# Kernel tuning notes

Hardware: AMD Instinct MI355X
Metric: run time of the kernel (lower is better)

## Reference

```python
import jax, jax.numpy as jnp
import numpy as np
from jax import lax

D_MODEL, D_STATE, D_CONV, EXPAND = 768, 16, 4, 2
D_INNER = EXPAND * D_MODEL          # 1536
DT_RANK = D_MODEL // 16             # 48
B_SZ, H_TOK, W_TOK = 2, 64, 32
L_SEQ = H_TOK * W_TOK               # 2048


def setup_inputs() -> dict:
    key = jax.random.key(0)
    ks = jax.random.split(key, 8)
    s = lambda k, shape: (jax.random.normal(k, shape, jnp.float32) * 0.02)
    A_log = jnp.log(jnp.tile(jnp.arange(1, D_STATE + 1, dtype=jnp.float32), (D_INNER, 1)))
    return {
        "x": jax.random.normal(ks[0], (B_SZ, L_SEQ, D_MODEL), jnp.float32),
        "ln_w": jnp.ones((D_MODEL,), jnp.float32),
        "ln_b": jnp.zeros((D_MODEL,), jnp.float32),
        "in_proj_w": s(ks[1], (2 * D_INNER, D_MODEL)),
        "conv_w": s(ks[2], (D_INNER, 1, D_CONV)),   # depthwise kernel [O, I/g=1, K]
        "conv_b": jnp.zeros((D_INNER,), jnp.float32),
        "x_proj_w": s(ks[3], (DT_RANK + 2 * D_STATE, D_INNER)),
        "dt_proj_w": s(ks[4], (D_INNER, DT_RANK)),
        "dt_proj_b": 0.01 * jax.random.normal(ks[5], (D_INNER,), jnp.float32),
        "A_log": A_log,
        "D_param": jnp.ones((D_INNER,), jnp.float32),
        "out_proj_w": s(ks[6], (D_MODEL, D_INNER)),
        "H": H_TOK,
        "W": W_TOK,
    }


def _layernorm(x, w, b, eps=1e-5):
    mu = jnp.mean(x, axis=-1, keepdims=True)
    var = jnp.mean(jnp.square(x - mu), axis=-1, keepdims=True)
    return (x - mu) * lax.rsqrt(var + eps) * w + b


def _mamba_forward(xn, in_proj_w, conv_w, conv_b, x_proj_w, dt_proj_w, dt_proj_b, A_log, D_param, out_proj_w):
    # in_proj and split into x / z gates, both [B, L, d_inner]
    xz = jnp.einsum('bld,ed->ble', xn, in_proj_w)
    x_in, z = jnp.split(xz, 2, axis=-1)

    # causal depthwise conv1d over time
    x_ch = jnp.transpose(x_in, (0, 2, 1))  # [B, d_inner, L]
    x_ch = lax.conv_general_dilated(
        x_ch, conv_w, window_strides=(1,), padding=[(D_CONV - 1, 0)],
        dimension_numbers=('NCH', 'OIH', 'NCH'), feature_group_count=D_INNER)
    x_ch = x_ch + conv_b[None, :, None]
    x_s = jax.nn.silu(jnp.transpose(x_ch, (0, 2, 1)))  # [B, L, d_inner]

    # input-dependent dt, B, C
    x_dbl = jnp.einsum('bld,ed->ble', x_s, x_proj_w)
    dt = x_dbl[..., :DT_RANK]
    B_ssm = x_dbl[..., DT_RANK:DT_RANK + D_STATE]      # [B, L, N]
    C_ssm = x_dbl[..., DT_RANK + D_STATE:]             # [B, L, N]
    dt = jax.nn.softplus(jnp.einsum('blr,dr->bld', dt, dt_proj_w) + dt_proj_b)  # [B, L, d_inner]

    A = -jnp.exp(A_log)                                # [d_inner, N]
    deltaA = jnp.exp(dt[..., None] * A)                # [B, L, d_inner, N]
    deltaBu = dt[..., None] * B_ssm[:, :, None, :] * x_s[..., None]

    def step(h, inputs):
        dA_t, dBu_t, c_t = inputs
        h = dA_t * h + dBu_t                           # [B, d_inner, N]
        y_t = jnp.einsum('bdn,bn->bd', h, c_t)
        return h, y_t

    h0 = jnp.zeros((xn.shape[0], D_INNER, D_STATE), xn.dtype)
    _, ys = lax.scan(step, h0, (jnp.transpose(deltaA, (1, 0, 2, 3)),
                                jnp.transpose(deltaBu, (1, 0, 2, 3)),
                                jnp.transpose(C_ssm, (1, 0, 2))))
    y = jnp.transpose(ys, (1, 0, 2)) + x_s * D_param   # skip via D
    y = y * jax.nn.silu(z)
    return jnp.einsum('ble,de->bld', y, out_proj_w)


def reference(x, ln_w, ln_b, in_proj_w, conv_w, conv_b, x_proj_w, dt_proj_w, dt_proj_b, A_log, D_param, out_proj_w, H, W):
    xn = _layernorm(x, ln_w, ln_b)
    out = _mamba_forward(xn, in_proj_w, conv_w, conv_b, x_proj_w, dt_proj_w, dt_proj_b, A_log, D_param, out_proj_w)
    return out
```

## Files before the change

### kernel.cpp

```cpp
#include <hip/hip_runtime.h>

#define DM   768
#define DI   1536
#define DS   16
#define DTR  48
#define BSZ  2
#define LSEQ 2048
#define BL   (BSZ*LSEQ)
#define NC   64
#define CL   (LSEQ/NC)
#define LOG2E 1.4426950408889634f
#define RLOG2E 0.6931471805599453f

typedef short bf16x8 __attribute__((ext_vector_type(8)));
typedef short short8 __attribute__((ext_vector_type(8)));
typedef float f32x4  __attribute__((ext_vector_type(4)));

static __device__ __forceinline__ unsigned short f2bf(float f){
  union { float f; unsigned u; } v; v.f = f;
  unsigned r = v.u + 0x7FFFu + ((v.u >> 16) & 1u);
  return (unsigned short)(r >> 16);
}
static __device__ __forceinline__ float bf2f(unsigned short s){
  union { unsigned u; float f; } v; v.u = ((unsigned)s) << 16;
  return v.f;
}
static __device__ __forceinline__ unsigned short f2h(float f){
  union { _Float16 h; unsigned short u; } v; v.h = (_Float16)f; return v.u;
}
static __device__ __forceinline__ float h2f(unsigned short u){
  union { unsigned short u; _Float16 h; } v; v.u = u; return (float)v.h;
}
static __device__ __forceinline__ float fexp2(float x){ return __builtin_amdgcn_exp2f(x); }
static __device__ __forceinline__ float flog2(float x){ return __builtin_amdgcn_logf(x); }
static __device__ __forceinline__ float frcp(float x){ return __builtin_amdgcn_rcpf(x); }

static __device__ __forceinline__ void gload_lds16(const unsigned short* g, unsigned short* l){
  __builtin_amdgcn_global_load_lds(
      (const __attribute__((address_space(1))) void*)g,
      (__attribute__((address_space(3))) void*)l, 16, 0, 0);
}

#define EE0 (3072*768)
#define EE1 (EE0 + 128*1536)
#define EE2 (EE1 + 1536*64)
#define EE3 (EE2 + 768*1536)
#define NPAD ((EE3 + 255)/256)
__global__ __launch_bounds__(256) void pad_ln(const float* __restrict__ s0,
    const float* __restrict__ s1, const float* __restrict__ s2, const float* __restrict__ s3,
    unsigned short* __restrict__ d0, unsigned short* __restrict__ d1,
    unsigned short* __restrict__ d2, unsigned short* __restrict__ d3,
    const float* __restrict__ x, const float* __restrict__ lw,
    const float* __restrict__ lb, unsigned short* __restrict__ xn){
  __shared__ float ls_[4], lss_[4];
  if (blockIdx.x < NPAD){
    int idx = blockIdx.x*256 + threadIdx.x;
    if (idx < EE0){
      d0[idx] = f2bf(s0[idx]);
    } else if (idx < EE1){
      int i = idx - EE0; int n = i / 1536, k = i % 1536;
      d1[i] = (n < 80) ? f2bf(s1[(size_t)n*1536 + k]) : (unsigned short)0;
    } else if (idx < EE2){
      int i = idx - EE1; int n = i >> 6, k = i & 63;
      d2[i] = (k < DTR) ? f2bf(s2[(size_t)n*DTR + k]) : (unsigned short)0;
    } else if (idx < EE3){
      int i = idx - EE2;
      d3[i] = f2bf(s3[i]);
    }
    return;
  }
  int row = blockIdx.x - NPAD;
  const float* xr = x + (size_t)row*DM;
  float v[3]; float s=0.f, ss=0.f;
#pragma unroll
  for (int i=0;i<3;i++){ v[i]=xr[threadIdx.x + i*256]; s+=v[i]; ss+=v[i]*v[i]; }
  for (int o=32;o>0;o>>=1){ s += __shfl_down(s,o); ss += __shfl_down(ss,o); }
  int wv = threadIdx.x>>6;
  if ((threadIdx.x&63)==0){ ls_[wv]=s; lss_[wv]=ss; }
  __syncthreads();
  s  = ls_[0]+ls_[1]+ls_[2]+ls_[3];
  ss = lss_[0]+lss_[1]+lss_[2]+lss_[3];
  float mu  = s*(1.f/DM);
  float var = ss*(1.f/DM) - mu*mu;
  float rs  = rsqrtf(var + 1e-5f);
#pragma unroll
  for (int i=0;i<3;i++){
    int j = threadIdx.x + i*256;
    xn[(size_t)row*DM + j] = f2bf((v[i]-mu)*rs*lw[j] + lb[j]);
  }
}

__global__ __launch_bounds__(512) void gemm256(const unsigned short* __restrict__ A,
    const unsigned short* __restrict__ W, unsigned short* __restrict__ outS0,
    unsigned short* __restrict__ outS1)
{
  const int K = DM;
  __shared__ unsigned short As[3][8192];
  __shared__ unsigned short Ws[3][8192];
  const int tid = threadIdx.x, lane = tid & 63, wave = tid >> 6;
  const int wm = wave >> 2, wn = wave & 3;
  const int m0 = blockIdx.y*256, n0 = blockIdx.x*256;
  const int srow = lane >> 2;
  const int gch  = (lane & 3) ^ (srow & 3);
  const unsigned short* gA0 = A + (size_t)(m0 + wave*16 + srow)*K + gch*8;
  const unsigned short* gW0 = W + (size_t)(n0 + wave*16 + srow)*K + gch*8;
  const int lo0 = (wave*64)*8;
  const int r = lane & 15, kb = lane >> 4;

  f32x4 acc[8][4];
#pragma unroll
  for (int i=0;i<8;i++)
#pragma unroll
    for (int j=0;j<4;j++){ f32x4 zv = {0.f,0.f,0.f,0.f}; acc[i][j] = zv; }

  int fAo[8], fWo[4];
#pragma unroll
  for (int mi=0;mi<8;mi++){ int rr = wm*128 + mi*16 + r; fAo[mi] = (rr*4 + (kb ^ (rr&3)))*8; }
#pragma unroll
  for (int ni=0;ni<4;ni++){ int rw = wn*64 + ni*16 + r; fWo[ni] = (rw*4 + (kb ^ (rw&3)))*8; }

  gload_lds16(gA0,                    &As[0][lo0]);
  gload_lds16(gA0 + (size_t)128*K,    &As[0][lo0 + 4096]);
  gload_lds16(gW0,                    &Ws[0][lo0]);
  gload_lds16(gW0 + (size_t)128*K,    &Ws[0][lo0 + 4096]);

  const int nt = K >> 5;
  int cur = 0, nxt = 1;
  for (int t=0; t<nt; ++t){
    if (t+1 < nt){
      const int ko = (t+1)*32;
      gload_lds16(gA0 + ko,                 &As[nxt][lo0]);
      gload_lds16(gA0 + ko + (size_t)128*K, &As[nxt][lo0 + 4096]);
      gload_lds16(gW0 + ko,                 &Ws[nxt][lo0]);
      gload_lds16(gW0 + ko + (size_t)128*K, &Ws[nxt][lo0 + 4096]);
      asm volatile("s_waitcnt vmcnt(4)" ::: "memory");
    } else {
      asm volatile("s_waitcnt vmcnt(0)" ::: "memory");
    }
    __builtin_amdgcn_s_barrier();
    __builtin_amdgcn_sched_barrier(0);
    bf16x8 af[8], bw[4];
#pragma unroll
    for (int i=0;i<8;i++) af[i] = *(const bf16x8*)(&As[cur][0] + fAo[i]);
#pragma unroll
    for (int i=0;i<4;i++) bw[i] = *(const bf16x8*)(&Ws[cur][0] + fWo[i]);
#pragma unroll
    for (int mi=0;mi<8;mi++)
#pragma unroll
      for (int ni=0;ni<4;ni++)
        acc[mi][ni] = __builtin_amdgcn_mfma_f32_16x16x32_bf16(af[mi], bw[ni], acc[mi][ni], 0,0,0);
    cur = nxt;
    nxt = (nxt == 2) ? 0 : nxt + 1;
  }
  const int cr = (lane>>4)*4, cc = lane & 15;
#pragma unroll
  for (int mi=0;mi<8;mi++)
#pragma unroll
  for (int ni=0;ni<4;ni++)
#pragma unroll
  for (int j=0;j<4;j++){
    int m = m0 + wm*128 + mi*16 + cr + j;
    int n = n0 + wn*64 + ni*16 + cc;
    float cval = acc[mi][ni][j];
    if (n < DI){
      outS0[(size_t)m*DI + n] = f2bf(cval);
    } else {
      float sv = cval * frcp(1.f + fexp2(-cval*LOG2E));
      outS1[(size_t)m*DI + (n-DI)] = f2bf(sv);
    }
  }
}

__global__ __launch_bounds__(256) void gemm_lds(const unsigned short* __restrict__ A,
    const unsigned short* __restrict__ W, int K, float* __restrict__ outF)
{
  __shared__ unsigned short As[3][4096];
  __shared__ unsigned short Ws[3][4096];
  const int tid = threadIdx.x, lane = tid & 63, wave = tid >> 6;
  const int wm = wave >> 1, wn = wave & 1;
  const int m0 = blockIdx.y*128, n0 = blockIdx.x*128;
  const int srow = lane >> 2;
  const int gch  = (lane & 3) ^ (srow & 3);
  const unsigned short* gA0 = A + (size_t)(m0 + wave*16 + srow)*K + gch*8;
  const unsigned short* gW0 = W + (size_t)(n0 + wave*16 + srow)*K + gch*8;
  const int lo = wave*512;
  const int r = lane & 15, kb = lane >> 4;
  const int fx = (kb ^ (r & 3))*8;
  const int fAo = (wm*64 + r)*32 + fx;
  const int fWo = (wn*64 + r)*32 + fx;

  f32x4 acc[4][4];
#pragma unroll
  for (int i=0;i<4;i++)
#pragma unroll
    for (int j=0;j<4;j++){ f32x4 zv = {0.f,0.f,0.f,0.f}; acc[i][j] = zv; }

  gload_lds16(gA0,                &As[0][lo]);
  gload_lds16(gA0 + (size_t)64*K, &As[0][2048+lo]);
  gload_lds16(gW0,                &Ws[0][lo]);
  gload_lds16(gW0 + (size_t)64*K, &Ws[0][2048+lo]);

  const int nt = K >> 5;
  int cur = 0, nxt = 1;
  for (int t=0; t<nt; ++t){
    if (t+1 < nt){
      const int ko = (t+1)*32;
      gload_lds16(gA0 + ko,                &As[nxt][lo]);
      gload_lds16(gA0 + ko + (size_t)64*K, &As[nxt][2048+lo]);
      gload_lds16(gW0 + ko,                &Ws[nxt][lo]);
      gload_lds16(gW0 + ko + (size_t)64*K, &Ws[nxt][2048+lo]);
      asm volatile("s_waitcnt vmcnt(4)" ::: "memory");
    } else {
      asm volatile("s_waitcnt vmcnt(0)" ::: "memory");
    }
    __builtin_amdgcn_s_barrier();
    __builtin_amdgcn_sched_barrier(0);
    const unsigned short* fA = &As[cur][0] + fAo;
    const unsigned short* fW = &Ws[cur][0] + fWo;
    bf16x8 af[4], bw[4];
#pragma unroll
    for (int i=0;i<4;i++) af[i] = *(const bf16x8*)(fA + i*512);
#pragma unroll
    for (int i=0;i<4;i++) bw[i] = *(const bf16x8*)(fW + i*512);
#pragma unroll
    for (int mi=0;mi<4;mi++)
#pragma unroll
      for (int ni=0;ni<4;ni++)
        acc[mi][ni] = __builtin_amdgcn_mfma_f32_16x16x32_bf16(af[mi], bw[ni], acc[mi][ni], 0,0,0);
    cur = nxt;
    nxt = (nxt == 2) ? 0 : nxt + 1;
  }
  const int cr = (lane>>4)*4, cc = lane & 15;
#pragma unroll
  for (int mi=0;mi<4;mi++)
#pragma unroll
  for (int ni=0;ni<4;ni++)
#pragma unroll
  for (int j=0;j<4;j++){
    int m = m0 + wm*64 + mi*16 + cr + j;
    int n = n0 + wn*64 + ni*16 + cc;
    outF[(size_t)m*DM + n] = acc[mi][ni][j];
  }
}

__global__ __launch_bounds__(256) void gemm_xdt(const unsigned short* __restrict__ A,
    const unsigned short* __restrict__ W, const unsigned short* __restrict__ Wdt,
    const float* __restrict__ bias, float* __restrict__ outF,
    unsigned short* __restrict__ dt_h)
{
  __shared__ unsigned short dtt[16][72];
  const int K = DI;
  const int lane = threadIdx.x & 63, wave = threadIdx.x >> 6;
  const int m0 = blockIdx.x*16;
  const int n0 = wave*32;
  const int r = lane & 15, kb = lane >> 4;
  const unsigned short* Ap = A + (size_t)(m0 + r)*K + kb*8;
  const unsigned short* Wp = W + (size_t)(n0 + r)*K + kb*8;
  f32x4 acc[2];
#pragma unroll
  for (int j=0;j<2;j++){ f32x4 zv = {0.f,0.f,0.f,0.f}; acc[j] = zv; }
  for (int k=0;k<K;k+=32){
    bf16x8 af = *(const bf16x8*)(Ap + k);
    bf16x8 bw0 = *(const bf16x8*)(Wp + k);
    bf16x8 bw1 = *(const bf16x8*)(Wp + (size_t)16*K + k);
    acc[0] = __builtin_amdgcn_mfma_f32_16x16x32_bf16(af, bw0, acc[0], 0,0,0);
    acc[1] = __builtin_amdgcn_mfma_f32_16x16x32_bf16(af, bw1, acc[1], 0,0,0);
  }
  const int cr = (lane>>4)*4, cc = lane & 15;
#pragma unroll
  for (int ni=0;ni<2;ni++)
#pragma unroll
  for (int j=0;j<4;j++){
    int m = m0 + cr + j;
    int n = n0 + ni*16 + cc;
    float v = acc[ni][j];
    outF[(size_t)m*128 + n] = v;
    if (n < 64)
      dtt[cr+j][n] = (n < DTR) ? f2bf(v) : (unsigned short)0;
  }
  __syncthreads();
  bf16x8 af2[2];
#pragma unroll
  for (int s=0;s<2;s++) af2[s] = *(const bf16x8*)(&dtt[r][s*32 + kb*8]);
#pragma unroll
  for (int nf=0; nf<24; nf++){
    int nb = wave*384 + nf*16;
    const unsigned short* wp = Wdt + (size_t)(nb + r)*64 + kb*8;
    bf16x8 b0 = *(const bf16x8*)(wp);
    bf16x8 b1 = *(const bf16x8*)(wp + 32);
    f32x4 a2 = {0.f,0.f,0.f,0.f};
    a2 = __builtin_amdgcn_mfma_f32_16x16x32_bf16(af2[0], b0, a2, 0,0,0);
    a2 = __builtin_amdgcn_mfma_f32_16x16x32_bf16(af2[1], b1, a2, 0,0,0);
    int n = nb + cc;
    float bn = bias[n];
#pragma unroll
    for (int j=0;j<4;j++){
      float q = a2[j] + bn;
      float sp = flog2(1.f + fexp2(q*LOG2E)) * RLOG2E;
      dt_h[(size_t)(m0 + cr + j)*DI + n] = f2h(sp);
    }
  }
}

__global__ __launch_bounds__(192) void conv_silu(const unsigned short* __restrict__ x_in,
    const float* __restrict__ cw, const float* __restrict__ cb,
    unsigned short* __restrict__ xs)
{
  const int lb = (blockIdx.x & 511)*4;
  const int b  = blockIdx.x >> 9;
  const int d8 = threadIdx.x * 8;
  f32x4 w[8];
#pragma unroll
  for (int dd=0;dd<8;dd++) w[dd] = *(const f32x4*)(cw + (d8+dd)*4);
  float cbv[8];
  {
    f32x4 c0 = *(const f32x4*)(cb + d8);
    f32x4 c1 = *(const f32x4*)(cb + d8 + 4);
#pragma unroll
    for (int dd=0;dd<4;dd++){ cbv[dd]=c0[dd]; cbv[4+dd]=c1[dd]; }
  }
  float xr[7][8];
#pragma unroll
  for (int rr=0; rr<7; rr++){
    int ls = lb - 3 + rr;
    if (ls >= 0){
      short8 xv = *(const short8*)(x_in + ((size_t)b*LSEQ + ls)*DI + d8);
#pragma unroll
      for (int dd=0;dd<8;dd++) xr[rr][dd] = bf2f((unsigned short)xv[dd]);
    } else {
#pragma unroll
      for (int dd=0;dd<8;dd++) xr[rr][dd] = 0.f;
    }
  }
#pragma unroll
  for (int j=0;j<4;j++){
    short8 o;
#pragma unroll
    for (int dd=0;dd<8;dd++){
      float a = cbv[dd] + w[dd][0]*xr[j][dd] + w[dd][1]*xr[j+1][dd]
                        + w[dd][2]*xr[j+2][dd] + w[dd][3]*xr[j+3][dd];
      float sv = a * frcp(1.f + fexp2(-a*LOG2E));
      o[dd] = (short)f2bf(sv);
    }
    *(short8*)(xs + ((size_t)b*LSEQ + lb + j)*DI + d8) = o;
  }
}

__global__ __launch_bounds__(256) void scan_p1(const unsigned short* __restrict__ dt_h,
    const unsigned short* __restrict__ xs, const float* __restrict__ xdbl,
    float* __restrict__ S, float* __restrict__ Et)
{
  __shared__ unsigned int dxs[CL*64];
  __shared__ float Bs[CL][16];
  const int d0 = blockIdx.x*64, c = blockIdx.y, b = blockIdx.z;
  const int tid = threadIdx.x;
  const int l0 = c*CL;
  {
    int rr = tid >> 3, dcol = (tid & 7)*8;
    size_t g = ((size_t)b*LSEQ + l0 + rr)*DI + d0 + dcol;
    short8 dv = *(const short8*)(dt_h + g);
    short8 xv = *(const short8*)(xs + g);
    unsigned int* dst = &dxs[rr*64 + dcol];
#pragma unroll
    for (int j=0;j<8;j++)
      dst[j] = ((unsigned)(unsigned short)xv[j] << 16) | (unsigned short)dv[j];
  }
#pragma unroll
  for (int it=0; it<2; it++){
    int ii = it*256 + tid; int rr = ii >> 4, cc2 = ii & 15;
    Bs[rr][cc2] = xdbl[((size_t)b*LSEQ + l0 + rr)*128 + 48 + cc2];
  }
  __syncthreads();
  const int dloc = tid >> 2, ng = tid & 3;
  float h0=0.f, h1=0.f, h2=0.f, h3=0.f;
  float sdt = 0.f;
  for (int t=0;t<CL;t++){
    unsigned int pk = dxs[t*64 + dloc];
    float dtv = h2f((unsigned short)(pk & 0xFFFFu));
    float xsv = bf2f((unsigned short)(pk >> 16));
    sdt += dtv;
    float dx = dtv*xsv;
    float E  = fexp2(-dtv*LOG2E);
    float E2 = E*E, E4 = E2*E2, E8 = E4*E4;
    float Eg = 1.f;
    if (ng & 1) Eg = E4;
    if (ng & 2) Eg *= E8;
    float e0 = Eg*E, e1 = e0*E, e2 = e0*E2, e3 = e1*E2;
    f32x4 Bq = *(const f32x4*)(&Bs[t][ng*4]);
    h0 = e0*h0 + dx*Bq[0];
    h1 = e1*h1 + dx*Bq[1];
    h2 = e2*h2 + dx*Bq[2];
    h3 = e3*h3 + dx*Bq[3];
  }
  const size_t bd = (size_t)b*DI + d0 + dloc;
  f32x4 sv = {h0,h1,h2,h3};
  *(f32x4*)(S + (bd*NC + c)*DS + ng*4) = sv;
  if (ng == 0) Et[bd*NC + c] = fexp2(-sdt*LOG2E);
}

__global__ __launch_bounds__(256) void scan_comb(const float* __restrict__ S,
    const float* __restrict__ Et, float* __restrict__ Hs){
  const int bd = blockIdx.x;
  const int n = threadIdx.x & 15, co = threadIdx.x >> 4;
  const int m = n + 1;
  __shared__ float PsL[16][17], SsL[16][17];
  const float* Sp = S + (size_t)bd*NC*DS;
  const float* Ep = Et + (size_t)bd*NC;
  float p[4], s[4];
#pragma unroll
  for (int j=0;j<4;j++){
    int cc = co*4 + j;
    float E = Ep[cc];
    float E2=E*E, E4=E2*E2, E8=E4*E4, E16=E8*E8;
    float pw = ((m&1)?E:1.f);
    pw *= ((m&2)?E2:1.f);
    pw *= ((m&4)?E4:1.f);
    pw *= ((m&8)?E8:1.f);
    pw *= ((m&16)?E16:1.f);
    p[j] = pw;
    s[j] = Sp[cc*DS + n];
  }
  float Pa=1.f, Sa=0.f;
#pragma unroll
  for (int j=0;j<4;j++){ Sa = p[j]*Sa + s[j]; Pa *= p[j]; }
  PsL[n][co] = Pa; SsL[n][co] = Sa;
  __syncthreads();
  if (threadIdx.x < 16){
    int nn = threadIdx.x;
    float h = 0.f;
#pragma unroll
    for (int q=0;q<16;q++){
      float P = PsL[nn][q], Sv = SsL[nn][q];
      SsL[nn][q] = h;
      h = P*h + Sv;
    }
  }
  __syncthreads();
  float h = SsL[n][co];
  float* Hp = Hs + (size_t)bd*NC*DS;
#pragma unroll
  for (int j=0;j<4;j++){
    int cc = co*4 + j;
    Hp[cc*DS + n] = h;
    h = p[j]*h + s[j];
  }
}

__global__ __launch_bounds__(256) void scan_p2(const unsigned short* __restrict__ dt_h,
    const unsigned short* __restrict__ xs, const unsigned short* __restrict__ z_bf,
    const float* __restrict__ xdbl, const float* __restrict__ Dp,
    const float* __restrict__ Hs, unsigned short* __restrict__ y_bf)
{
  __shared__ unsigned int dxs[CL*64];
  __shared__ unsigned short zss[CL*64];
  __shared__ unsigned short ys[CL*64];
  __shared__ float Bs[CL][16];
  __shared__ float Cs[CL][16];
  const int d0 = blockIdx.x*64, c = blockIdx.y, b = blockIdx.z;
  const int tid = threadIdx.x;
  const int l0 = c*CL;
  {
    int rr = tid >> 3, dcol = (tid & 7)*8;
    size_t g = ((size_t)b*LSEQ + l0 + rr)*DI + d0 + dcol;
    short8 dv = *(const short8*)(dt_h + g);
    short8 xv = *(const short8*)(xs + g);
    *(short8*)(&zss[rr*64 + dcol]) = *(const short8*)(z_bf + g);
    unsigned int* dst = &dxs[rr*64 + dcol];
#pragma unroll
    for (int j=0;j<8;j++)
      dst[j] = ((unsigned)(unsigned short)xv[j] << 16) | (unsigned short)dv[j];
  }
#pragma unroll
  for (int it=0; it<2; it++){
    int ii = it*256 + tid; int rr = ii >> 4, cc2 = ii & 15;
    const float* xr = xdbl + ((size_t)b*LSEQ + l0 + rr)*128;
    Bs[rr][cc2] = xr[48+cc2];
    Cs[rr][cc2] = xr[64+cc2];
  }
  __syncthreads();
  const int dloc = tid >> 2, ng = tid & 3;
  const size_t bd = (size_t)b*DI + d0 + dloc;
  float h0,h1,h2,h3;
  {
    f32x4 hv = *(const f32x4*)(Hs + (bd*NC + c)*DS + ng*4);
    h0=hv[0]; h1=hv[1]; h2=hv[2]; h3=hv[3];
  }
  const float dpar = Dp[d0 + dloc];
  for (int t=0;t<CL;t++){
    unsigned int pk = dxs[t*64 + dloc];
    float dtv = h2f((unsigned short)(pk & 0xFFFFu));
    float xsv = bf2f((unsigned short)(pk >> 16));
    float dx = dtv*xsv;
    float E  = fexp2(-dtv*LOG2E);
    float E2 = E*E, E4 = E2*E2, E8 = E4*E4;
    float Eg = 1.f;
    if (ng & 1) Eg = E4;
    if (ng & 2) Eg *= E8;
    float e0 = Eg*E, e1 = e0*E, e2 = e0*E2, e3 = e1*E2;
    f32x4 Bq = *(const f32x4*)(&Bs[t][ng*4]);
    f32x4 Cq = *(const f32x4*)(&Cs[t][ng*4]);
    h0 = e0*h0 + dx*Bq[0];
    h1 = e1*h1 + dx*Bq[1];
    h2 = e2*h2 + dx*Bq[2];
    h3 = e3*h3 + dx*Bq[3];
    float y = (h0*Cq[0] + h1*Cq[1]) + (h2*Cq[2] + h3*Cq[3]);
    y += __shfl_xor(y, 1);
    y += __shfl_xor(y, 2);
    if (ng == 0){
      float sg = bf2f(zss[t*64 + dloc]);
      float yg = (y + xsv*dpar) * sg;
      ys[t*64 + dloc] = f2bf(yg);
    }
  }
  __syncthreads();
  {
    int fi = tid*8;
    int rr = fi >> 6, dcol = fi & 63;
    *(short8*)(y_bf + ((size_t)b*LSEQ + l0 + rr)*DI + d0 + dcol) = *(const short8*)(&ys[fi]);
  }
}

extern "C" void kernel_launch(void* const* d_in, const int* in_sizes, int n_in,
                              void* d_out, int out_size, void* d_ws, size_t ws_size,
                              hipStream_t stream) {
  const float* x       = (const float*)d_in[0];
  const float* ln_w    = (const float*)d_in[1];
  const float* ln_b    = (const float*)d_in[2];
  const float* in_w    = (const float*)d_in[3];
  const float* conv_w  = (const float*)d_in[4];
  const float* conv_b  = (const float*)d_in[5];
  const float* xproj_w = (const float*)d_in[6];
  const float* dt_w    = (const float*)d_in[7];
  const float* dt_b    = (const float*)d_in[8];
  const float* D_param = (const float*)d_in[10];
  const float* out_w   = (const float*)d_in[11];
  float* out = (float*)d_out;
  (void)in_sizes; (void)n_in; (void)out_size; (void)ws_size;

  char* ws = (char*)d_ws;
  size_t off = 0;
  auto alloc = [&](size_t bytes)->void*{
    void* p = ws + off; off += (bytes + 255) & ~(size_t)255; return p;
  };
  unsigned short* W_in  = (unsigned short*)alloc((size_t)3072*768*2);
  unsigned short* W_x   = (unsigned short*)alloc((size_t)128*1536*2);
  unsigned short* W_dt  = (unsigned short*)alloc((size_t)1536*64*2);
  unsigned short* W_out = (unsigned short*)alloc((size_t)768*1536*2);
  unsigned short* xn    = (unsigned short*)alloc((size_t)BL*DM*2);
  unsigned short* x_in  = (unsigned short*)alloc((size_t)BL*DI*2);
  unsigned short* z_bf  = (unsigned short*)alloc((size_t)BL*DI*2);
  unsigned short* xs    = (unsigned short*)alloc((size_t)BL*DI*2);
  unsigned short* dt_h  = (unsigned short*)alloc((size_t)BL*DI*2);
  float*          x_dbl = (float*)alloc((size_t)BL*128*4);
  float*          S     = (float*)alloc((size_t)BSZ*DI*NC*DS*4);
  float*          Hs    = (float*)alloc((size_t)BSZ*DI*NC*DS*4);
  float* Et = (float*)xn;
  unsigned short* y_bf = x_in;

  pad_ln<<<NPAD + BL, 256, 0, stream>>>(in_w, xproj_w, dt_w, out_w,
                                        W_in, W_x, W_dt, W_out, x, ln_w, ln_b, xn);

  gemm256<<<dim3(3072/256, BL/256), 512, 0, stream>>>(xn, W_in, x_in, z_bf);

  conv_silu<<<BL/4, 192, 0, stream>>>(x_in, conv_w, conv_b, xs);

  gemm_xdt<<<BL/16, 256, 0, stream>>>(xs, W_x, W_dt, dt_b, x_dbl, dt_h);

  scan_p1<<<dim3(DI/64, NC, BSZ), 256, 0, stream>>>(dt_h, xs, x_dbl, S, Et);
  scan_comb<<<BSZ*DI, 256, 0, stream>>>(S, Et, Hs);
  scan_p2<<<dim3(DI/64, NC, BSZ), 256, 0, stream>>>(dt_h, xs, z_bf, x_dbl, D_param, Hs, y_bf);

  gemm_lds<<<dim3(DM/128, BL/128), 256, 0, stream>>>(y_bf, W_out, 1536, out);
}
```

Measured before the change: 165.4 us.

## Fuse chunked scan passes into one kernel with decoupled look-back flags

Replaces the three-kernel chunked selective scan (local chunk pass, cross-chunk combine, second pass) with a single kernel. Each block publishes its chunk-local state and summed dt to a global aggregate buffer, raises an atomic flag, then spins on the flags of all earlier chunks and serially combines their states before running the output pass. This drops two launches and the reload of dt/xs/B from global memory, in exchange for spin-waiting that depends on earlier chunks being scheduled first. Later chunks redo up to 63 combine steps each, and a memset of the flags is added.

New measurement: 464.1 us. 181% more time.

```diff
diff --git a/kernel.cpp b/kernel.cpp
--- a/kernel.cpp
+++ b/kernel.cpp
@@ -9,6 +9,8 @@
 #define BL   (BSZ*LSEQ)
 #define NC   64
 #define CL   (LSEQ/NC)
+#define NDT  24
+#define NREC 1088
 #define LOG2E 1.4426950408889634f
 #define RLOG2E 0.6931471805599453f
 
@@ -346,13 +348,19 @@
   }
 }
 
-__global__ __launch_bounds__(256) void scan_p1(const unsigned short* __restrict__ dt_h,
-    const unsigned short* __restrict__ xs, const float* __restrict__ xdbl,
-    float* __restrict__ S, float* __restrict__ Et)
+__global__ __launch_bounds__(256) void scan_fused(const unsigned short* __restrict__ dt_h,
+    const unsigned short* __restrict__ xs, const unsigned short* __restrict__ z_bf,
+    const float* __restrict__ xdbl, const float* __restrict__ Dp,
+    float* __restrict__ agg, int* __restrict__ flags,
+    unsigned short* __restrict__ y_bf)
 {
   __shared__ unsigned int dxs[CL*64];
+  __shared__ unsigned short zss[CL*64];
+  __shared__ unsigned short ys[CL*64];
   __shared__ float Bs[CL][16];
-  const int d0 = blockIdx.x*64, c = blockIdx.y, b = blockIdx.z;
+  __shared__ float Cs[CL][16];
+  const int dtile = blockIdx.x, c = blockIdx.y, b = blockIdx.z;
+  const int d0 = dtile*64;
   const int tid = threadIdx.x;
   const int l0 = c*CL;
   {
@@ -360,6 +368,7 @@
     size_t g = ((size_t)b*LSEQ + l0 + rr)*DI + d0 + dcol;
     short8 dv = *(const short8*)(dt_h + g);
     short8 xv = *(const short8*)(xs + g);
+    *(short8*)(&zss[rr*64 + dcol]) = *(const short8*)(z_bf + g);
     unsigned int* dst = &dxs[rr*64 + dcol];
 #pragma unroll
     for (int j=0;j<8;j++)
@@ -368,12 +377,13 @@
 #pragma unroll
   for (int it=0; it<2; it++){
     int ii = it*256 + tid; int rr = ii >> 4, cc2 = ii & 15;
-    Bs[rr][cc2] = xdbl[((size_t)b*LSEQ + l0 + rr)*128 + 48 + cc2];
+    const float* xrp = xdbl + ((size_t)b*LSEQ + l0 + rr)*128;
+    Bs[rr][cc2] = xrp[48+cc2];
+    Cs[rr][cc2] = xrp[64+cc2];
   }
   __syncthreads();
   const int dloc = tid >> 2, ng = tid & 3;
-  float h0=0.f, h1=0.f, h2=0.f, h3=0.f;
-  float sdt = 0.f;
+  float h0=0.f, h1=0.f, h2=0.f, h3=0.f, sdt=0.f;
   for (int t=0;t<CL;t++){
     unsigned int pk = dxs[t*64 + dloc];
     float dtv = h2f((unsigned short)(pk & 0xFFFFu));
@@ -392,99 +402,41 @@
     h2 = e2*h2 + dx*Bq[2];
     h3 = e3*h3 + dx*Bq[3];
   }
-  const size_t bd = (size_t)b*DI + d0 + dloc;
-  f32x4 sv = {h0,h1,h2,h3};
-  *(f32x4*)(S + (bd*NC + c)*DS + ng*4) = sv;
-  if (ng == 0) Et[bd*NC + c] = fexp2(-sdt*LOG2E);
-}
-
-__global__ __launch_bounds__(256) void scan_comb(const float* __restrict__ S,
-    const float* __restrict__ Et, float* __restrict__ Hs){
-  const int bd = blockIdx.x;
-  const int n = threadIdx.x & 15, co = threadIdx.x >> 4;
-  const int m = n + 1;
-  __shared__ float PsL[16][17], SsL[16][17];
-  const float* Sp = S + (size_t)bd*NC*DS;
-  const float* Ep = Et + (size_t)bd*NC;
-  float p[4], s[4];
-#pragma unroll
-  for (int j=0;j<4;j++){
-    int cc = co*4 + j;
-    float E = Ep[cc];
-    float E2=E*E, E4=E2*E2, E8=E4*E4, E16=E8*E8;
-    float pw = ((m&1)?E:1.f);
-    pw *= ((m&2)?E2:1.f);
-    pw *= ((m&4)?E4:1.f);
-    pw *= ((m&8)?E8:1.f);
-    pw *= ((m&16)?E16:1.f);
-    p[j] = pw;
-    s[j] = Sp[cc*DS + n];
-  }
-  float Pa=1.f, Sa=0.f;
-#pragma unroll
-  for (int j=0;j<4;j++){ Sa = p[j]*Sa + s[j]; Pa *= p[j]; }
-  PsL[n][co] = Pa; SsL[n][co] = Sa;
+  {
+    float* rec = agg + ((size_t)(b*NC + c)*NDT + dtile)*NREC;
+    f32x4 sv = {h0,h1,h2,h3};
+    *(f32x4*)(rec + dloc*16 + ng*4) = sv;
+    if (ng == 0) rec[1024 + dloc] = sdt;
+  }
   __syncthreads();
-  if (threadIdx.x < 16){
-    int nn = threadIdx.x;
-    float h = 0.f;
-#pragma unroll
-    for (int q=0;q<16;q++){
-      float P = PsL[nn][q], Sv = SsL[nn][q];
-      SsL[nn][q] = h;
-      h = P*h + Sv;
-    }
-  }
-  __syncthreads();
-  float h = SsL[n][co];
-  float* Hp = Hs + (size_t)bd*NC*DS;
-#pragma unroll
-  for (int j=0;j<4;j++){
-    int cc = co*4 + j;
-    Hp[cc*DS + n] = h;
-    h = p[j]*h + s[j];
-  }
-}
-
-__global__ __launch_bounds__(256) void scan_p2(const unsigned short* __restrict__ dt_h,
-    const unsigned short* __restrict__ xs, const unsigned short* __restrict__ z_bf,
-    const float* __restrict__ xdbl, const float* __restrict__ Dp,
-    const float* __restrict__ Hs, unsigned short* __restrict__ y_bf)
-{
-  __shared__ unsigned int dxs[CL*64];
-  __shared__ unsigned short zss[CL*64];
-  __shared__ unsigned short ys[CL*64];
-  __shared__ float Bs[CL][16];
-  __shared__ float Cs[CL][16];
-  const int d0 = blockIdx.x*64, c = blockIdx.y, b = blockIdx.z;
-  const int tid = threadIdx.x;
-  const int l0 = c*CL;
-  {
-    int rr = tid >> 3, dcol = (tid & 7)*8;
-    size_t g = ((size_t)b*LSEQ + l0 + rr)*DI + d0 + dcol;
-    short8 dv = *(const short8*)(dt_h + g);
-    short8 xv = *(const short8*)(xs + g);
-    *(short8*)(&zss[rr*64 + dcol]) = *(const short8*)(z_bf + g);
-    unsigned int* dst = &dxs[rr*64 + dcol];
-#pragma unroll
-    for (int j=0;j<8;j++)
-      dst[j] = ((unsigned)(unsigned short)xv[j] << 16) | (unsigned short)dv[j];
-  }
-#pragma unroll
-  for (int it=0; it<2; it++){
-    int ii = it*256 + tid; int rr = ii >> 4, cc2 = ii & 15;
-    const float* xr = xdbl + ((size_t)b*LSEQ + l0 + rr)*128;
-    Bs[rr][cc2] = xr[48+cc2];
-    Cs[rr][cc2] = xr[64+cc2];
-  }
-  __syncthreads();
-  const int dloc = tid >> 2, ng = tid & 3;
-  const size_t bd = (size_t)b*DI + d0 + dloc;
-  float h0,h1,h2,h3;
-  {
-    f32x4 hv = *(const f32x4*)(Hs + (bd*NC + c)*DS + ng*4);
-    h0=hv[0]; h1=hv[1]; h2=hv[2]; h3=hv[3];
-  }
+  if (tid == 0)
+    __hip_atomic_fetch_add(&flags[(b*NC + c)*NDT + dtile], 1,
+                           __ATOMIC_RELEASE, __HIP_MEMORY_SCOPE_AGENT);
+  float g0=0.f, g1=0.f, g2=0.f, g3=0.f;
+  if (c > 0){
+    for (int j = tid; j < c; j += 256){
+      while (__hip_atomic_fetch_add(&flags[(b*NC + j)*NDT + dtile], 0,
+                                    __ATOMIC_RELAXED, __HIP_MEMORY_SCOPE_AGENT) == 0) {}
+    }
+    __syncthreads();
+    __threadfence();
+    for (int j=0; j<c; j++){
+      const float* rec = agg + ((size_t)(b*NC + j)*NDT + dtile)*NREC;
+      float sj = rec[1024 + dloc];
+      f32x4 Sj = *(const f32x4*)(rec + dloc*16 + ng*4);
+      float E  = fexp2(-sj*LOG2E);
+      float E2 = E*E, E4 = E2*E2, E8 = E4*E4;
+      float Eg = 1.f;
+      if (ng & 1) Eg = E4;
+      if (ng & 2) Eg *= E8;
+      float e0 = Eg*E, e1 = e0*E, e2 = e0*E2, e3 = e1*E2;
+      g0 = e0*g0 + Sj[0];
+      g1 = e1*g1 + Sj[1];
+      g2 = e2*g2 + Sj[2];
+      g3 = e3*g3 + Sj[3];
+    }
+  }
+  h0=g0; h1=g1; h2=g2; h3=g3;
   const float dpar = Dp[d0 + dloc];
   for (int t=0;t<CL;t++){
     unsigned int pk = dxs[t*64 + dloc];
@@ -552,10 +504,11 @@
   unsigned short* xs    = (unsigned short*)alloc((size_t)BL*DI*2);
   unsigned short* dt_h  = (unsigned short*)alloc((size_t)BL*DI*2);
   float*          x_dbl = (float*)alloc((size_t)BL*128*4);
-  float*          S     = (float*)alloc((size_t)BSZ*DI*NC*DS*4);
-  float*          Hs    = (float*)alloc((size_t)BSZ*DI*NC*DS*4);
-  float* Et = (float*)xn;
+  float*          agg   = (float*)alloc((size_t)BSZ*NC*NDT*NREC*4);
+  int*            flags = (int*)alloc((size_t)BSZ*NC*NDT*4);
   unsigned short* y_bf = x_in;
+
+  hipMemsetAsync(flags, 0, (size_t)BSZ*NC*NDT*4, stream);
 
   pad_ln<<<NPAD + BL, 256, 0, stream>>>(in_w, xproj_w, dt_w, out_w,
                                         W_in, W_x, W_dt, W_out, x, ln_w, ln_b, xn);
@@ -566,9 +519,8 @@
 
   gemm_xdt<<<BL/16, 256, 0, stream>>>(xs, W_x, W_dt, dt_b, x_dbl, dt_h);
 
-  scan_p1<<<dim3(DI/64, NC, BSZ), 256, 0, stream>>>(dt_h, xs, x_dbl, S, Et);
-  scan_comb<<<BSZ*DI, 256, 0, stream>>>(S, Et, Hs);
-  scan_p2<<<dim3(DI/64, NC, BSZ), 256, 0, stream>>>(dt_h, xs, z_bf, x_dbl, D_param, Hs, y_bf);
+  scan_fused<<<dim3(NDT, NC, BSZ), 256, 0, stream>>>(dt_h, xs, z_bf, x_dbl,
+                                                     D_param, agg, flags, y_bf);
 
   gemm_lds<<<dim3(DM/128, BL/128), 256, 0, stream>>>(y_bf, W_out, 1536, out);
 }
```
